# Kernel optimization log

Measured on AMD Instinct MI355X. Metric: run time of the kernel, lower is better.

The kernel has to match this reference:

```python
import jax, jax.numpy as jnp
import numpy as np

B, SQ, SK, D, H = 8, 2048, 2048, 512, 8
QP, KP, VP = 512, 512, 4096  # VP must equal D*H for O_w to accept the concat


def setup_inputs() -> dict:
    key = jax.random.key(0)
    ks = jax.random.split(key, 9)
    q_in = jax.random.normal(ks[0], (B, SQ, D), dtype=jnp.float32)
    k_in = jax.random.normal(ks[1], (B, SK, D), dtype=jnp.float32)
    v_in = jax.random.normal(ks[2], (B, SK, D), dtype=jnp.float32)
    mask = jax.random.randint(ks[3], (B, SQ, SK), 0, 2, dtype=jnp.int32)
    W_q = jax.random.normal(ks[4], (D, QP), dtype=jnp.float32) * 0.02
    W_k = jax.random.normal(ks[5], (D, KP), dtype=jnp.float32) * 0.02
    W_v = jax.random.normal(ks[6], (D, VP), dtype=jnp.float32) * 0.02
    W_o = jax.random.normal(ks[7], (VP, D), dtype=jnp.float32) * 0.02
    b_o = jnp.zeros((D,), dtype=jnp.float32)
    return {"q_in": q_in, "k_in": k_in, "v_in": v_in,
            "W_q": W_q, "W_k": W_k, "W_v": W_v, "W_o": W_o, "b_o": b_o,
            "mask": mask}


def reference(q_in, k_in, v_in, W_q, W_k, W_v, W_o, b_o, mask):
    b, sq, d = q_in.shape
    sk = k_in.shape[1]
    # NOTE: original scales by sqrt(input_dim // num_heads), NOT actual head dim
    scale = jnp.asarray(np.sqrt(d // H), dtype=q_in.dtype)
    q = q_in @ W_q  # (B, Sq, QP)
    k = k_in @ W_k  # (B, Sk, KP)
    v = v_in @ W_v  # (B, Sk, VP)
    q_h = q.reshape(b, sq, H, -1).transpose(0, 2, 1, 3)  # (B,H,Sq,dq)
    k_h = k.reshape(b, sk, H, -1).transpose(0, 2, 1, 3)  # (B,H,Sk,dk)
    v_h = v.reshape(b, sk, H, -1).transpose(0, 2, 1, 3)  # (B,H,Sk,dv)
    attn = jnp.einsum('bhid,bhkd->bhik', q_h, k_h)  # (B,H,Sq,Sk)
    attn = jnp.where(mask[:, None, :, :] == 0, jnp.asarray(-1e9, attn.dtype), attn)
    attn = jax.nn.softmax(attn / scale, axis=-1)
    out = attn @ v_h  # (B,H,Sq,dv)
    # Faithful to original bug: transpose(0,1) swaps BATCH and HEAD, then reshape
    out = jnp.transpose(out, (1, 0, 2, 3)).reshape(b, sq, -1)  # (B,Sq,H*dv)
    return out @ W_o + b_o
```

## Files before the change

### kernel.cpp

```cpp
#include <hip/hip_runtime.h>
#include <math.h>

typedef __bf16 bf16x8 __attribute__((ext_vector_type(8)));
typedef float fx4 __attribute__((ext_vector_type(4)));
typedef unsigned short u16;
typedef unsigned short u16x8 __attribute__((ext_vector_type(8)));
typedef unsigned int u32;

__device__ __forceinline__ fx4 mfma16(bf16x8 a, bf16x8 b, fx4 c) {
  return __builtin_amdgcn_mfma_f32_16x16x32_bf16(a, b, c, 0, 0, 0);
}
__device__ __forceinline__ u16 f2bf(float f) {
  u32 u = __float_as_uint(f);
  u += 0x7fffu + ((u >> 16) & 1u);
  return (u16)(u >> 16);
}

#define BB 8
#define SS 2048
#define DD 512
#define HH 8
#define DQ 64
#define DV 512
#define VP 4096

#define OFF_QP  ((size_t)0)
#define OFF_KP  ((size_t)16777216)
#define OFF_WQT ((size_t)33554432)
#define OFF_WKT ((size_t)34078720)
#define OFF_WVT ((size_t)34603008)
#define OFF_WOT ((size_t)38797312)
#define OFF_VT  ((size_t)76546048)
#define OFF_XB  ((size_t)210763776)

__global__ __launch_bounds__(256) void transpose_w(const float* __restrict__ W,
                                                   u16* __restrict__ Wt,
                                                   int K, int N) {
  __shared__ float t[32][33];
  const int n0 = blockIdx.x * 32, k0 = blockIdx.y * 32;
  const int tx = threadIdx.x & 31, ty = threadIdx.x >> 5;
#pragma unroll
  for (int i = 0; i < 32; i += 8)
    t[ty + i][tx] = W[(size_t)(k0 + ty + i) * N + n0 + tx];
  __syncthreads();
#pragma unroll
  for (int i = 0; i < 32; i += 8)
    Wt[(size_t)(n0 + ty + i) * K + k0 + tx] = f2bf(t[tx][ty + i]);
}

template <int AFP32, int EPI>
__global__ __launch_bounds__(256) void gemm_bt(const void* __restrict__ Ap,
                                               const u16* __restrict__ Bt,
                                               void* __restrict__ Cp,
                                               int M, int N, int K,
                                               const float* __restrict__ bias,
                                               float scale) {
  __shared__ union {
    struct { u16 As[128 * 32]; u16 Bs[128 * 32]; } s;
    u16 T[4][64 * 68];
  } sm;
  const int tid = threadIdx.x;
  const int lane = tid & 63, w = tid >> 6;
  const int lhi = lane >> 4, llo = lane & 15;
  const int wm = w >> 1, wn = w & 1;
  const int m0 = blockIdx.y * 128, n0 = blockIdx.x * 128;

  fx4 acc[4][4];
#pragma unroll
  for (int i = 0; i < 4; ++i)
#pragma unroll
    for (int j = 0; j < 4; ++j) acc[i][j] = (fx4){0.f, 0.f, 0.f, 0.f};

  for (int k0 = 0; k0 < K; k0 += 32) {
    if (AFP32) {
      const float* A = (const float*)Ap;
      const int row = tid >> 1, co = (tid & 1) * 16;
      const float* src = A + (size_t)(m0 + row) * K + k0 + co;
      float4 v0 = *(const float4*)(src + 0);
      float4 v1 = *(const float4*)(src + 4);
      float4 v2 = *(const float4*)(src + 8);
      float4 v3 = *(const float4*)(src + 12);
      u16x8 p0 = {f2bf(v0.x), f2bf(v0.y), f2bf(v0.z), f2bf(v0.w),
                  f2bf(v1.x), f2bf(v1.y), f2bf(v1.z), f2bf(v1.w)};
      u16x8 p1 = {f2bf(v2.x), f2bf(v2.y), f2bf(v2.z), f2bf(v2.w),
                  f2bf(v3.x), f2bf(v3.y), f2bf(v3.z), f2bf(v3.w)};
      *(u16x8*)&sm.s.As[row * 32 + co] = p0;
      *(u16x8*)&sm.s.As[row * 32 + co + 8] = p1;
    } else {
      const u16* A = (const u16*)Ap;
#pragma unroll
      for (int j = 0; j < 2; ++j) {
        int cc = j * 256 + tid;
        int row = cc >> 2, c8 = (cc & 3) * 8;
        *(uint4*)&sm.s.As[cc * 8] = *(const uint4*)&A[(size_t)(m0 + row) * K + k0 + c8];
      }
    }
#pragma unroll
    for (int j = 0; j < 2; ++j) {
      int cc = j * 256 + tid;
      int row = cc >> 2, c8 = (cc & 3) * 8;
      *(uint4*)&sm.s.Bs[cc * 8] = *(const uint4*)&Bt[(size_t)(n0 + row) * K + k0 + c8];
    }
    __syncthreads();
    bf16x8 af[4], bfv[4];
#pragma unroll
    for (int mi = 0; mi < 4; ++mi)
      af[mi] = *(const bf16x8*)&sm.s.As[(wm * 64 + mi * 16 + llo) * 32 + lhi * 8];
#pragma unroll
    for (int ni = 0; ni < 4; ++ni)
      bfv[ni] = *(const bf16x8*)&sm.s.Bs[(wn * 64 + ni * 16 + llo) * 32 + lhi * 8];
#pragma unroll
    for (int mi = 0; mi < 4; ++mi)
#pragma unroll
      for (int ni = 0; ni < 4; ++ni)
        acc[mi][ni] = mfma16(af[mi], bfv[ni], acc[mi][ni]);
    __syncthreads();
  }

  const int rbase = m0 + wm * 64, cbase = n0 + wn * 64;
  if (EPI == 0) {
    u16* C = (u16*)Cp;
#pragma unroll
    for (int mi = 0; mi < 4; ++mi) {
      int r0 = rbase + mi * 16 + lhi * 4;
#pragma unroll
      for (int ni = 0; ni < 4; ++ni) {
        int c = cbase + ni * 16 + llo;
#pragma unroll
        for (int r = 0; r < 4; ++r)
          C[(size_t)(r0 + r) * N + c] = f2bf(acc[mi][ni][r] * scale);
      }
    }
  } else if (EPI == 1) {
    u16* Tw = &sm.T[w][0];
#pragma unroll
    for (int mi = 0; mi < 4; ++mi)
#pragma unroll
      for (int ni = 0; ni < 4; ++ni) {
        ushort4 pk;
        pk.x = f2bf(acc[mi][ni][0]);
        pk.y = f2bf(acc[mi][ni][1]);
        pk.z = f2bf(acc[mi][ni][2]);
        pk.w = f2bf(acc[mi][ni][3]);
        *(ushort4*)&Tw[(ni * 16 + llo) * 68 + mi * 16 + lhi * 4] = pk;
      }
    u16* VtC = (u16*)Cp;
    const int bsel = rbase >> 11;
    const int sb = rbase & 2047;
    u16* dst = VtC + ((size_t)(bsel * VP + cbase + lane)) * SS + sb;
#pragma unroll
    for (int j = 0; j < 8; ++j) {
      u16x8 vv = *(u16x8*)&Tw[lane * 68 + j * 8];
      *(u16x8*)&dst[j * 8] = vv;
    }
  } else {
    float* C = (float*)Cp;
#pragma unroll
    for (int ni = 0; ni < 4; ++ni) {
      int c = cbase + ni * 16 + llo;
      float bv = bias[c];
#pragma unroll
      for (int mi = 0; mi < 4; ++mi) {
        int r0 = rbase + mi * 16 + lhi * 4;
#pragma unroll
        for (int r = 0; r < 4; ++r)
          C[(size_t)(r0 + r) * N + c] = acc[mi][ni][r] + bv;
      }
    }
  }
}

#define SM_S 68
__global__ __launch_bounds__(256, 2) void attn(const u16* __restrict__ Qp,
                                               const u16* __restrict__ Kp,
                                               const u16* __restrict__ Vt,
                                               const int* __restrict__ mask,
                                               u16* __restrict__ Xb) {
  const int lin = blockIdx.x;
  const int xcd = lin & 7, idx = lin >> 3;
  const int bh = xcd * 8 + (idx >> 5);
  const int qt = idx & 31;
  const int b = bh & 7, h = bh >> 3;
  const int m0 = qt * 64;
  const int tid = threadIdx.x, w = tid >> 6, lane = tid & 63;
  const int lhi = lane >> 4, llo = lane & 15;

  __shared__ float Ssm[64 * SM_S];
  __shared__ u16 Psm[64 * SM_S];
  __shared__ float sm_l[64];

  bf16x8 qf[4][2];
#pragma unroll
  for (int mt = 0; mt < 4; ++mt)
#pragma unroll
    for (int ks = 0; ks < 2; ++ks)
      qf[mt][ks] = *(const bf16x8*)&Qp[(size_t)(b * SS + m0 + mt * 16 + llo) * 512 +
                                       h * DQ + ks * 32 + lhi * 8];

  fx4 acc[4][8];
#pragma unroll
  for (int mt = 0; mt < 4; ++mt)
#pragma unroll
    for (int nt = 0; nt < 8; ++nt) acc[mt][nt] = (fx4){0.f, 0.f, 0.f, 0.f};

  const int r8 = tid >> 3, c8 = (tid & 7) * 8;
  const int* mrow0 = mask + (size_t)(b * SS + m0 + r8) * SS;
  const int* mrow1 = mrow0 + 32 * SS;
  float ls0 = 0.f, ls1 = 0.f;

  const int colw = w * 16 + llo;
  const size_t kbase = (size_t)(b * SS) * 512 + h * DQ + lhi * 8;

  for (int n0 = 0; n0 < SS; n0 += 64) {
    bf16x8 kf0 = *(const bf16x8*)&Kp[kbase + (size_t)(n0 + colw) * 512];
    bf16x8 kf1 = *(const bf16x8*)&Kp[kbase + (size_t)(n0 + colw) * 512 + 32];
    int4 ma0 = *(const int4*)&mrow0[n0 + c8];
    int4 ma1 = *(const int4*)&mrow0[n0 + c8 + 4];
    int4 mb0 = *(const int4*)&mrow1[n0 + c8];
    int4 mb1 = *(const int4*)&mrow1[n0 + c8 + 4];

#pragma unroll
    for (int mt = 0; mt < 4; ++mt) {
      fx4 s = (fx4){0.f, 0.f, 0.f, 0.f};
      s = mfma16(qf[mt][0], kf0, s);
      s = mfma16(qf[mt][1], kf1, s);
#pragma unroll
      for (int r = 0; r < 4; ++r)
        Ssm[(mt * 16 + lhi * 4 + r) * SM_S + colw] = s[r];
    }
    __syncthreads();

#pragma unroll
    for (int half = 0; half < 2; ++half) {
      const int rr = r8 + half * 32;
      const int4 mv0 = half ? mb0 : ma0;
      const int4 mv1 = half ? mb1 : ma1;
      float4 xa = *(const float4*)&Ssm[rr * SM_S + c8];
      float4 xb = *(const float4*)&Ssm[rr * SM_S + c8 + 4];
      float x0 = mv0.x ? xa.x : -1.25e8f;
      float x1 = mv0.y ? xa.y : -1.25e8f;
      float x2 = mv0.z ? xa.z : -1.25e8f;
      float x3 = mv0.w ? xa.w : -1.25e8f;
      float x4 = mv1.x ? xb.x : -1.25e8f;
      float x5 = mv1.y ? xb.y : -1.25e8f;
      float x6 = mv1.z ? xb.z : -1.25e8f;
      float x7 = mv1.w ? xb.w : -1.25e8f;
      float p0 = __expf(x0), p1 = __expf(x1), p2 = __expf(x2), p3 = __expf(x3);
      float p4 = __expf(x4), p5 = __expf(x5), p6 = __expf(x6), p7 = __expf(x7);
      u16x8 pb = {f2bf(p0), f2bf(p1), f2bf(p2), f2bf(p3),
                  f2bf(p4), f2bf(p5), f2bf(p6), f2bf(p7)};
      *(u16x8*)&Psm[rr * SM_S + c8] = pb;
      float ps = ((p0 + p1) + (p2 + p3)) + ((p4 + p5) + (p6 + p7));
      if (half) ls1 += ps; else ls0 += ps;
    }
    __syncthreads();

    bf16x8 pf[4][2];
#pragma unroll
    for (int mt = 0; mt < 4; ++mt)
#pragma unroll
      for (int kk = 0; kk < 2; ++kk)
        pf[mt][kk] = *(const bf16x8*)&Psm[(mt * 16 + llo) * SM_S + kk * 32 + lhi * 8];
#pragma unroll
    for (int nt = 0; nt < 8; ++nt) {
      const size_t vrow =
          (size_t)(b * VP + h * DV + w * 128 + nt * 16 + llo) * SS + n0 + lhi * 8;
      bf16x8 vf0 = *(const bf16x8*)&Vt[vrow];
      bf16x8 vf1 = *(const bf16x8*)&Vt[vrow + 32];
#pragma unroll
      for (int mt = 0; mt < 4; ++mt) {
        fx4 a = acc[mt][nt];
        a = mfma16(pf[mt][0], vf0, a);
        a = mfma16(pf[mt][1], vf1, a);
        acc[mt][nt] = a;
      }
    }
  }

  ls0 += __shfl_xor(ls0, 1); ls0 += __shfl_xor(ls0, 2); ls0 += __shfl_xor(ls0, 4);
  ls1 += __shfl_xor(ls1, 1); ls1 += __shfl_xor(ls1, 2); ls1 += __shfl_xor(ls1, 4);
  if ((tid & 7) == 0) { sm_l[r8] = ls0; sm_l[r8 + 32] = ls1; }
  __syncthreads();

  float linv[4][4];
#pragma unroll
  for (int mt = 0; mt < 4; ++mt)
#pragma unroll
    for (int r = 0; r < 4; ++r) linv[mt][r] = 1.0f / sm_l[mt * 16 + lhi * 4 + r];

  u16* Xs = (u16*)Ssm;
  const int er = tid >> 4, ec = (tid & 15) * 32;
#pragma unroll
  for (int mt = 0; mt < 4; ++mt) {
#pragma unroll
    for (int nt = 0; nt < 8; ++nt)
#pragma unroll
      for (int r = 0; r < 4; ++r)
        Xs[(lhi * 4 + r) * 520 + w * 128 + nt * 16 + llo] =
            f2bf(acc[mt][nt][r] * linv[mt][r]);
    __syncthreads();
    {
      const u16* src = Xs + er * 520 + ec;
      u16* dst = Xb + (size_t)((h * 8 + b) * SS + m0 + mt * 16 + er) * 512 + ec;
      uint4 a0 = *(const uint4*)(src + 0);
      uint4 a1 = *(const uint4*)(src + 8);
      uint4 a2 = *(const uint4*)(src + 16);
      uint4 a3 = *(const uint4*)(src + 24);
      *(uint4*)(dst + 0) = a0;
      *(uint4*)(dst + 8) = a1;
      *(uint4*)(dst + 16) = a2;
      *(uint4*)(dst + 24) = a3;
    }
    __syncthreads();
  }
}

extern "C" void kernel_launch(void* const* d_in, const int* in_sizes, int n_in,
                              void* d_out, int out_size, void* d_ws, size_t ws_size,
                              hipStream_t stream) {
  (void)in_sizes; (void)n_in; (void)out_size; (void)ws_size;
  const float* q_in = (const float*)d_in[0];
  const float* k_in = (const float*)d_in[1];
  const float* v_in = (const float*)d_in[2];
  const float* W_q  = (const float*)d_in[3];
  const float* W_k  = (const float*)d_in[4];
  const float* W_v  = (const float*)d_in[5];
  const float* W_o  = (const float*)d_in[6];
  const float* b_o  = (const float*)d_in[7];
  const int*   mask = (const int*)d_in[8];

  char* ws = (char*)d_ws;
  u16* Qp   = (u16*)(ws + OFF_QP);
  u16* Kp   = (u16*)(ws + OFF_KP);
  u16* Wqt  = (u16*)(ws + OFF_WQT);
  u16* Wkt  = (u16*)(ws + OFF_WKT);
  u16* Wvt  = (u16*)(ws + OFF_WVT);
  u16* Wot  = (u16*)(ws + OFF_WOT);
  u16* Vt   = (u16*)(ws + OFF_VT);
  u16* Xb   = (u16*)(ws + OFF_XB);

  transpose_w<<<dim3(16, 16), 256, 0, stream>>>(W_q, Wqt, 512, 512);
  transpose_w<<<dim3(16, 16), 256, 0, stream>>>(W_k, Wkt, 512, 512);
  transpose_w<<<dim3(128, 16), 256, 0, stream>>>(W_v, Wvt, 512, 4096);
  transpose_w<<<dim3(16, 128), 256, 0, stream>>>(W_o, Wot, 4096, 512);

  gemm_bt<1, 0><<<dim3(4, 128), 256, 0, stream>>>(q_in, Wqt, Qp, 16384, 512, 512, nullptr, 0.125f);
  gemm_bt<1, 0><<<dim3(4, 128), 256, 0, stream>>>(k_in, Wkt, Kp, 16384, 512, 512, nullptr, 1.0f);
  gemm_bt<1, 1><<<dim3(32, 128), 256, 0, stream>>>(v_in, Wvt, Vt, 16384, 4096, 512, nullptr, 1.0f);

  attn<<<dim3(2048), 256, 0, stream>>>(Qp, Kp, Vt, mask, Xb);

  gemm_bt<0, 2><<<dim3(4, 128), 256, 0, stream>>>(Xb, Wot, d_out, 16384, 512, 4096, b_o, 1.0f);
}
```

Measured before the change: 1.373 ms.

## Split attention over value halves, pack mask to bytes, widen key tile, use exp2

Adds a mask_pack kernel that turns the int32 mask into bytes, so the attention kernel reads a quarter of the mask traffic. The attention grid is doubled, with each block covering half of the 512-wide value dimension. This halves accumulator registers per block, at the cost of computing QK^T and softmax twice. The key tile grows from 64 to 128, the Q scale absorbs log2(e) so the kernel can use the hardware exp2, and s_setprio is raised around the PV MFMAs. The extra mask-pack pass and the redundant score work are the added costs.

Result: no change. 1.392 ms (+1.4%).

```diff
diff --git a/kernel.cpp b/kernel.cpp
--- a/kernel.cpp
+++ b/kernel.cpp
@@ -6,6 +6,7 @@
 typedef unsigned short u16;
 typedef unsigned short u16x8 __attribute__((ext_vector_type(8)));
 typedef unsigned int u32;
+typedef unsigned char u8;
 
 __device__ __forceinline__ fx4 mfma16(bf16x8 a, bf16x8 b, fx4 c) {
   return __builtin_amdgcn_mfma_f32_16x16x32_bf16(a, b, c, 0, 0, 0);
@@ -15,6 +16,7 @@
   u += 0x7fffu + ((u >> 16) & 1u);
   return (u16)(u >> 16);
 }
+__device__ __forceinline__ float ex2(float x) { return __builtin_amdgcn_exp2f(x); }
 
 #define BB 8
 #define SS 2048
@@ -30,6 +32,7 @@
 #define OFF_WKT ((size_t)34078720)
 #define OFF_WVT ((size_t)34603008)
 #define OFF_WOT ((size_t)38797312)
+#define OFF_MB  ((size_t)42991616)
 #define OFF_VT  ((size_t)76546048)
 #define OFF_XB  ((size_t)210763776)
 
@@ -46,6 +49,21 @@
 #pragma unroll
   for (int i = 0; i < 32; i += 8)
     Wt[(size_t)(n0 + ty + i) * K + k0 + tx] = f2bf(t[tx][ty + i]);
+}
+
+__global__ __launch_bounds__(256) void mask_pack(const int* __restrict__ m,
+                                                 u8* __restrict__ mb) {
+  const size_t i = ((size_t)blockIdx.x * 256 + threadIdx.x) * 16;
+  int4 a0 = *(const int4*)(m + i);
+  int4 a1 = *(const int4*)(m + i + 4);
+  int4 a2 = *(const int4*)(m + i + 8);
+  int4 a3 = *(const int4*)(m + i + 12);
+  uint4 o;
+  o.x = (a0.x ? 1u : 0u) | ((a0.y ? 1u : 0u) << 8) | ((a0.z ? 1u : 0u) << 16) | ((a0.w ? 1u : 0u) << 24);
+  o.y = (a1.x ? 1u : 0u) | ((a1.y ? 1u : 0u) << 8) | ((a1.z ? 1u : 0u) << 16) | ((a1.w ? 1u : 0u) << 24);
+  o.z = (a2.x ? 1u : 0u) | ((a2.y ? 1u : 0u) << 8) | ((a2.z ? 1u : 0u) << 16) | ((a2.w ? 1u : 0u) << 24);
+  o.w = (a3.x ? 1u : 0u) | ((a3.y ? 1u : 0u) << 8) | ((a3.z ? 1u : 0u) << 16) | ((a3.w ? 1u : 0u) << 24);
+  *(uint4*)(mb + i) = o;
 }
 
 template <int AFP32, int EPI>
@@ -170,23 +188,23 @@
   }
 }
 
-#define SM_S 68
+#define KB 128
+#define SMS 132
 __global__ __launch_bounds__(256, 2) void attn(const u16* __restrict__ Qp,
                                                const u16* __restrict__ Kp,
                                                const u16* __restrict__ Vt,
-                                               const int* __restrict__ mask,
+                                               const u8* __restrict__ mb,
                                                u16* __restrict__ Xb) {
   const int lin = blockIdx.x;
   const int xcd = lin & 7, idx = lin >> 3;
-  const int bh = xcd * 8 + (idx >> 5);
-  const int qt = idx & 31;
-  const int b = bh & 7, h = bh >> 3;
+  const int chunk = idx >> 5, qt = idx & 31;
+  const int b = chunk >> 1, dvh = chunk & 1, h = xcd;
   const int m0 = qt * 64;
   const int tid = threadIdx.x, w = tid >> 6, lane = tid & 63;
   const int lhi = lane >> 4, llo = lane & 15;
 
-  __shared__ float Ssm[64 * SM_S];
-  __shared__ u16 Psm[64 * SM_S];
+  __shared__ float Ssm[64 * SMS];
+  __shared__ u16 Psm[64 * SMS];
   __shared__ float sm_l[64];
 
   bf16x8 qf[4][2];
@@ -197,83 +215,100 @@
       qf[mt][ks] = *(const bf16x8*)&Qp[(size_t)(b * SS + m0 + mt * 16 + llo) * 512 +
                                        h * DQ + ks * 32 + lhi * 8];
 
-  fx4 acc[4][8];
+  fx4 acc[4][4];
 #pragma unroll
   for (int mt = 0; mt < 4; ++mt)
 #pragma unroll
-    for (int nt = 0; nt < 8; ++nt) acc[mt][nt] = (fx4){0.f, 0.f, 0.f, 0.f};
-
-  const int r8 = tid >> 3, c8 = (tid & 7) * 8;
-  const int* mrow0 = mask + (size_t)(b * SS + m0 + r8) * SS;
-  const int* mrow1 = mrow0 + 32 * SS;
+    for (int nt = 0; nt < 4; ++nt) acc[mt][nt] = (fx4){0.f, 0.f, 0.f, 0.f};
+
+  const int r8 = tid >> 3, c16 = (tid & 7) * 16;
+  const u8* mr0 = mb + (size_t)(b * SS + m0 + r8) * SS;
+  const u8* mr1 = mr0 + 32 * SS;
   float ls0 = 0.f, ls1 = 0.f;
 
-  const int colw = w * 16 + llo;
+  const int cw = w * 32;
   const size_t kbase = (size_t)(b * SS) * 512 + h * DQ + lhi * 8;
-
-  for (int n0 = 0; n0 < SS; n0 += 64) {
-    bf16x8 kf0 = *(const bf16x8*)&Kp[kbase + (size_t)(n0 + colw) * 512];
-    bf16x8 kf1 = *(const bf16x8*)&Kp[kbase + (size_t)(n0 + colw) * 512 + 32];
-    int4 ma0 = *(const int4*)&mrow0[n0 + c8];
-    int4 ma1 = *(const int4*)&mrow0[n0 + c8 + 4];
-    int4 mb0 = *(const int4*)&mrow1[n0 + c8];
-    int4 mb1 = *(const int4*)&mrow1[n0 + c8 + 4];
-
-#pragma unroll
-    for (int mt = 0; mt < 4; ++mt) {
-      fx4 s = (fx4){0.f, 0.f, 0.f, 0.f};
-      s = mfma16(qf[mt][0], kf0, s);
-      s = mfma16(qf[mt][1], kf1, s);
-#pragma unroll
-      for (int r = 0; r < 4; ++r)
-        Ssm[(mt * 16 + lhi * 4 + r) * SM_S + colw] = s[r];
-    }
+  const size_t vbase =
+      (size_t)(b * VP + h * DV + dvh * 256 + w * 64 + llo) * SS + lhi * 8;
+
+  for (int n0 = 0; n0 < SS; n0 += KB) {
+    bf16x8 kf[2][2];
+#pragma unroll
+    for (int ct = 0; ct < 2; ++ct)
+#pragma unroll
+      for (int ks = 0; ks < 2; ++ks)
+        kf[ct][ks] = *(const bf16x8*)&Kp[kbase +
+                                         (size_t)(n0 + cw + ct * 16 + llo) * 512 +
+                                         ks * 32];
+    uint4 ma0 = *(const uint4*)&mr0[n0 + c16];
+    uint4 ma1 = *(const uint4*)&mr1[n0 + c16];
+
+#pragma unroll
+    for (int ct = 0; ct < 2; ++ct)
+#pragma unroll
+      for (int mt = 0; mt < 4; ++mt) {
+        fx4 s = (fx4){0.f, 0.f, 0.f, 0.f};
+        s = mfma16(qf[mt][0], kf[ct][0], s);
+        s = mfma16(qf[mt][1], kf[ct][1], s);
+#pragma unroll
+        for (int r = 0; r < 4; ++r)
+          Ssm[(mt * 16 + lhi * 4 + r) * SMS + cw + ct * 16 + llo] = s[r];
+      }
     __syncthreads();
 
 #pragma unroll
     for (int half = 0; half < 2; ++half) {
       const int rr = r8 + half * 32;
-      const int4 mv0 = half ? mb0 : ma0;
-      const int4 mv1 = half ? mb1 : ma1;
-      float4 xa = *(const float4*)&Ssm[rr * SM_S + c8];
-      float4 xb = *(const float4*)&Ssm[rr * SM_S + c8 + 4];
-      float x0 = mv0.x ? xa.x : -1.25e8f;
-      float x1 = mv0.y ? xa.y : -1.25e8f;
-      float x2 = mv0.z ? xa.z : -1.25e8f;
-      float x3 = mv0.w ? xa.w : -1.25e8f;
-      float x4 = mv1.x ? xb.x : -1.25e8f;
-      float x5 = mv1.y ? xb.y : -1.25e8f;
-      float x6 = mv1.z ? xb.z : -1.25e8f;
-      float x7 = mv1.w ? xb.w : -1.25e8f;
-      float p0 = __expf(x0), p1 = __expf(x1), p2 = __expf(x2), p3 = __expf(x3);
-      float p4 = __expf(x4), p5 = __expf(x5), p6 = __expf(x6), p7 = __expf(x7);
-      u16x8 pb = {f2bf(p0), f2bf(p1), f2bf(p2), f2bf(p3),
+      const uint4 mv = half ? ma1 : ma0;
+      const float* Sr = &Ssm[rr * SMS + c16];
+      float4 xa = *(const float4*)(Sr + 0);
+      float4 xb = *(const float4*)(Sr + 4);
+      float4 xc = *(const float4*)(Sr + 8);
+      float4 xd = *(const float4*)(Sr + 12);
+      const float NEG = -1.0e9f;
+      float p0 = ex2((mv.x & 0x000000ffu) ? xa.x : NEG);
+      float p1 = ex2((mv.x & 0x0000ff00u) ? xa.y : NEG);
+      float p2 = ex2((mv.x & 0x00ff0000u) ? xa.z : NEG);
+      float p3 = ex2((mv.x & 0xff000000u) ? xa.w : NEG);
+      float p4 = ex2((mv.y & 0x000000ffu) ? xb.x : NEG);
+      float p5 = ex2((mv.y & 0x0000ff00u) ? xb.y : NEG);
+      float p6 = ex2((mv.y & 0x00ff0000u) ? xb.z : NEG);
+      float p7 = ex2((mv.y & 0xff000000u) ? xb.w : NEG);
+      float p8 = ex2((mv.z & 0x000000ffu) ? xc.x : NEG);
+      float p9 = ex2((mv.z & 0x0000ff00u) ? xc.y : NEG);
+      float p10 = ex2((mv.z & 0x00ff0000u) ? xc.z : NEG);
+      float p11 = ex2((mv.z & 0xff000000u) ? xc.w : NEG);
+      float p12 = ex2((mv.w & 0x000000ffu) ? xd.x : NEG);
+      float p13 = ex2((mv.w & 0x0000ff00u) ? xd.y : NEG);
+      float p14 = ex2((mv.w & 0x00ff0000u) ? xd.z : NEG);
+      float p15 = ex2((mv.w & 0xff000000u) ? xd.w : NEG);
+      u16x8 qa = {f2bf(p0), f2bf(p1), f2bf(p2), f2bf(p3),
                   f2bf(p4), f2bf(p5), f2bf(p6), f2bf(p7)};
-      *(u16x8*)&Psm[rr * SM_S + c8] = pb;
-      float ps = ((p0 + p1) + (p2 + p3)) + ((p4 + p5) + (p6 + p7));
+      u16x8 qb = {f2bf(p8), f2bf(p9), f2bf(p10), f2bf(p11),
+                  f2bf(p12), f2bf(p13), f2bf(p14), f2bf(p15)};
+      *(u16x8*)&Psm[rr * SMS + c16] = qa;
+      *(u16x8*)&Psm[rr * SMS + c16 + 8] = qb;
+      float ps = (((p0 + p1) + (p2 + p3)) + ((p4 + p5) + (p6 + p7))) +
+                 (((p8 + p9) + (p10 + p11)) + ((p12 + p13) + (p14 + p15)));
       if (half) ls1 += ps; else ls0 += ps;
     }
     __syncthreads();
 
-    bf16x8 pf[4][2];
-#pragma unroll
-    for (int mt = 0; mt < 4; ++mt)
-#pragma unroll
-      for (int kk = 0; kk < 2; ++kk)
-        pf[mt][kk] = *(const bf16x8*)&Psm[(mt * 16 + llo) * SM_S + kk * 32 + lhi * 8];
-#pragma unroll
-    for (int nt = 0; nt < 8; ++nt) {
-      const size_t vrow =
-          (size_t)(b * VP + h * DV + w * 128 + nt * 16 + llo) * SS + n0 + lhi * 8;
-      bf16x8 vf0 = *(const bf16x8*)&Vt[vrow];
-      bf16x8 vf1 = *(const bf16x8*)&Vt[vrow + 32];
-#pragma unroll
-      for (int mt = 0; mt < 4; ++mt) {
-        fx4 a = acc[mt][nt];
-        a = mfma16(pf[mt][0], vf0, a);
-        a = mfma16(pf[mt][1], vf1, a);
-        acc[mt][nt] = a;
-      }
+#pragma unroll
+    for (int kk = 0; kk < 4; ++kk) {
+      bf16x8 pf[4];
+#pragma unroll
+      for (int mt = 0; mt < 4; ++mt)
+        pf[mt] = *(const bf16x8*)&Psm[(mt * 16 + llo) * SMS + kk * 32 + lhi * 8];
+      __builtin_amdgcn_s_setprio(1);
+#pragma unroll
+      for (int nt = 0; nt < 4; ++nt) {
+        bf16x8 vf = *(const bf16x8*)&Vt[vbase + (size_t)(nt * 16) * SS + n0 + kk * 32];
+#pragma unroll
+        for (int mt = 0; mt < 4; ++mt)
+          acc[mt][nt] = mfma16(pf[mt], vf, acc[mt][nt]);
+      }
+      __builtin_amdgcn_s_setprio(0);
     }
   }
 
@@ -289,27 +324,24 @@
     for (int r = 0; r < 4; ++r) linv[mt][r] = 1.0f / sm_l[mt * 16 + lhi * 4 + r];
 
   u16* Xs = (u16*)Ssm;
-  const int er = tid >> 4, ec = (tid & 15) * 32;
+  const int er = tid >> 4, ec = (tid & 15) * 16;
 #pragma unroll
   for (int mt = 0; mt < 4; ++mt) {
 #pragma unroll
-    for (int nt = 0; nt < 8; ++nt)
+    for (int nt = 0; nt < 4; ++nt)
 #pragma unroll
       for (int r = 0; r < 4; ++r)
-        Xs[(lhi * 4 + r) * 520 + w * 128 + nt * 16 + llo] =
+        Xs[(lhi * 4 + r) * 264 + w * 64 + nt * 16 + llo] =
             f2bf(acc[mt][nt][r] * linv[mt][r]);
     __syncthreads();
     {
-      const u16* src = Xs + er * 520 + ec;
-      u16* dst = Xb + (size_t)((h * 8 + b) * SS + m0 + mt * 16 + er) * 512 + ec;
+      const u16* src = Xs + er * 264 + ec;
+      u16* dst = Xb + (size_t)((h * 8 + b) * SS + m0 + mt * 16 + er) * 512 +
+                 dvh * 256 + ec;
       uint4 a0 = *(const uint4*)(src + 0);
       uint4 a1 = *(const uint4*)(src + 8);
-      uint4 a2 = *(const uint4*)(src + 16);
-      uint4 a3 = *(const uint4*)(src + 24);
       *(uint4*)(dst + 0) = a0;
       *(uint4*)(dst + 8) = a1;
-      *(uint4*)(dst + 16) = a2;
-      *(uint4*)(dst + 24) = a3;
     }
     __syncthreads();
   }
@@ -336,6 +368,7 @@
   u16* Wkt  = (u16*)(ws + OFF_WKT);
   u16* Wvt  = (u16*)(ws + OFF_WVT);
   u16* Wot  = (u16*)(ws + OFF_WOT);
+  u8*  Mb   = (u8*)(ws + OFF_MB);
   u16* Vt   = (u16*)(ws + OFF_VT);
   u16* Xb   = (u16*)(ws + OFF_XB);
 
@@ -343,12 +376,13 @@
   transpose_w<<<dim3(16, 16), 256, 0, stream>>>(W_k, Wkt, 512, 512);
   transpose_w<<<dim3(128, 16), 256, 0, stream>>>(W_v, Wvt, 512, 4096);
   transpose_w<<<dim3(16, 128), 256, 0, stream>>>(W_o, Wot, 4096, 512);
-
-  gemm_bt<1, 0><<<dim3(4, 128), 256, 0, stream>>>(q_in, Wqt, Qp, 16384, 512, 512, nullptr, 0.125f);
+  mask_pack<<<dim3(8192), 256, 0, stream>>>(mask, Mb);
+
+  gemm_bt<1, 0><<<dim3(4, 128), 256, 0, stream>>>(q_in, Wqt, Qp, 16384, 512, 512, nullptr, 0.18033688011112f);
   gemm_bt<1, 0><<<dim3(4, 128), 256, 0, stream>>>(k_in, Wkt, Kp, 16384, 512, 512, nullptr, 1.0f);
   gemm_bt<1, 1><<<dim3(32, 128), 256, 0, stream>>>(v_in, Wvt, Vt, 16384, 4096, 512, nullptr, 1.0f);
 
-  attn<<<dim3(2048), 256, 0, stream>>>(Qp, Kp, Vt, mask, Xb);
+  attn<<<dim3(4096), 256, 0, stream>>>(Qp, Kp, Vt, Mb, Xb);
 
   gemm_bt<0, 2><<<dim3(4, 128), 256, 0, stream>>>(Xb, Wot, d_out, 16384, 512, 4096, b_o, 1.0f);
 }
```
